# Kernel tuning notes

Measured on AMD Instinct MI355X. Metric: run time of the kernel, lower is better.

The kernel has to match this reference:

```python
import jax, jax.numpy as jnp
import numpy as np

B, T, C, H = 4, 2048, 512, 8
HS = C // H  # head_size = 64
EPS = 1e-5


def layernorm(x, g, b):
    mu = jnp.mean(x, axis=-1, keepdims=True)
    var = jnp.mean(jnp.square(x - mu), axis=-1, keepdims=True)
    return (x - mu) * jax.lax.rsqrt(var + EPS) * g + b


def setup_inputs() -> dict:
    key = jax.random.key(0)
    ks = jax.random.split(key, 12)
    s_attn = 1.0 / np.sqrt(C)
    s_ff1 = 1.0 / np.sqrt(C)
    s_ff2 = 1.0 / np.sqrt(4 * C)
    return {
        "x": jax.random.normal(ks[0], (B, T, C), jnp.float32),
        "wq": jax.random.normal(ks[1], (H, C, HS), jnp.float32) * s_attn,
        "wk": jax.random.normal(ks[2], (H, C, HS), jnp.float32) * s_attn,
        "wv": jax.random.normal(ks[3], (H, C, HS), jnp.float32) * s_attn,
        "w1": jax.random.normal(ks[4], (C, 4 * C), jnp.float32) * s_ff1,
        "b1": jnp.zeros((4 * C,), jnp.float32),
        "w2": jax.random.normal(ks[5], (4 * C, C), jnp.float32) * s_ff2,
        "b2": jnp.zeros((C,), jnp.float32),
        "ln1_g": jnp.ones((C,), jnp.float32),
        "ln1_b": jnp.zeros((C,), jnp.float32),
        "ln2_g": jnp.ones((C,), jnp.float32),
        "ln2_b": jnp.zeros((C,), jnp.float32),
    }


def reference(x, wq, wk, wv, w1, b1, w2, b2, ln1_g, ln1_b, ln2_g, ln2_b):
    # pre-LN multi-head causal self-attention
    h = layernorm(x, ln1_g, ln1_b)                       # [B,T,C]
    q = jnp.einsum("btc,hcd->bhtd", h, wq)
    k = jnp.einsum("btc,hcd->bhtd", h, wk)
    v = jnp.einsum("btc,hcd->bhtd", h, wv)
    # NOTE: source scales by full embed dim C, not head_size
    scores = jnp.einsum("bhtd,bhsd->bhts", q, k) * (C ** -0.5)  # [B,H,T,T]
    causal = jnp.tril(jnp.ones((T, T), bool))
    scores = jnp.where(causal, scores, -jnp.inf)
    att = jax.nn.softmax(scores, axis=-1)
    out = jnp.einsum("bhts,bhsd->bhtd", att, v)          # [B,H,T,HS]
    out = out.transpose(0, 2, 1, 3).reshape(B, T, C)     # concat heads
    x = x + out
    # FFN with residual
    h2 = layernorm(x, ln2_g, ln2_b)
    ff = jax.nn.relu(h2 @ w1 + b1) @ w2 + b2
    return x + ff
```

## Files before the change

kernel.cpp:

```cpp
#include <hip/hip_runtime.h>

typedef unsigned short ushort_t;
typedef __attribute__((ext_vector_type(8))) short short8;
typedef __attribute__((ext_vector_type(4))) float floatx4;

#define B_  4
#define T_  2048
#define C_  512
#define H_  8
#define HS_ 64
#define M_  (B_*T_)
#define SCALE2 0.06376140168547404f

__device__ __forceinline__ float b2f(ushort_t u) {
  union { unsigned int i; float f; } w; w.i = ((unsigned int)u) << 16; return w.f;
}
__device__ __forceinline__ ushort_t f2b(float f) {
  union { float f; unsigned int i; } w; w.f = f;
  unsigned int x = w.i;
  return (ushort_t)((x + 0x7fffu + ((x >> 16) & 1u)) >> 16);
}
__device__ __forceinline__ ushort_t f2b_fast(float f) {
  union { float f; unsigned int i; } w; w.f = f;
  return (ushort_t)((w.i + 0x8000u) >> 16);
}
__device__ __forceinline__ void gl_lds16(const ushort_t* g, ushort_t* l) {
  __builtin_amdgcn_global_load_lds((const unsigned int*)g, (unsigned int*)l, 16, 0, 0);
}

__global__ __launch_bounds__(256) void transpose_all(const float* __restrict__ wq,
                                                     const float* __restrict__ wk,
                                                     const float* __restrict__ wv,
                                                     const float* __restrict__ w1,
                                                     const float* __restrict__ w2,
                                                     ushort_t* __restrict__ qkvt,
                                                     ushort_t* __restrict__ w1t,
                                                     ushort_t* __restrict__ w2t) {
  __shared__ ushort_t t[32][33];
  int idx = blockIdx.x;
  const float* in; ushort_t* out; int K, N, bx, by, z = 0;
  if (idx < 768) {
    int seg = idx >> 8, li = idx & 255;
    in = seg == 0 ? wq : (seg == 1 ? wk : wv);
    out = qkvt + (size_t)seg * 262144;
    K = 512; N = 64;
    z = li >> 5; li &= 31;
    bx = li & 1; by = li >> 1;
  } else if (idx < 1792) {
    int li = idx - 768;
    in = w1; out = w1t; K = 512; N = 2048;
    bx = li & 63; by = li >> 6;
  } else {
    int li = idx - 1792;
    in = w2; out = w2t; K = 2048; N = 512;
    bx = li & 15; by = li >> 4;
  }
  size_t zoff = (size_t)z * K * N;
  int n0 = bx * 32, k0 = by * 32;
  int tx = threadIdx.x & 31, ty = threadIdx.x >> 5;
#pragma unroll
  for (int i = 0; i < 4; i++)
    t[ty + 8 * i][tx] = f2b(in[zoff + (size_t)(k0 + ty + 8 * i) * N + n0 + tx]);
  __syncthreads();
#pragma unroll
  for (int i = 0; i < 4; i++)
    out[zoff + (size_t)(n0 + ty + 8 * i) * K + k0 + tx] = t[tx][ty + 8 * i];
}

__global__ __launch_bounds__(256) void ln_k(const float* __restrict__ X,
                                            const float* __restrict__ g,
                                            const float* __restrict__ bb,
                                            ushort_t* __restrict__ Y) {
  int wave = threadIdx.x >> 6, lane = threadIdx.x & 63;
  size_t row = (size_t)blockIdx.x * 4 + wave;
  float v[8], s = 0.f, s2 = 0.f;
#pragma unroll
  for (int i = 0; i < 8; i++) {
    float x = X[row * C_ + lane + 64 * i];
    v[i] = x; s += x; s2 += x * x;
  }
#pragma unroll
  for (int off = 32; off >= 1; off >>= 1) {
    s += __shfl_xor(s, off); s2 += __shfl_xor(s2, off);
  }
  float mu = s * (1.0f / C_);
  float var = s2 * (1.0f / C_) - mu * mu;
  float rs = rsqrtf(var + 1e-5f);
  ushort_t* yr = Y + row * C_;
#pragma unroll
  for (int i = 0; i < 8; i++) {
    int c = lane + 64 * i;
    yr[c] = f2b((v[i] - mu) * rs * g[c] + bb[c]);
  }
}

__global__ __launch_bounds__(256) void gemm_bt128(const ushort_t* __restrict__ A,
                                                  const ushort_t* __restrict__ Bt,
                                                  ushort_t* __restrict__ Out,
                                                  int K, int ldOut,
                                                  const float* __restrict__ bias,
                                                  int relu) {
  __shared__ __align__(16) ushort_t As[128 * 64];
  __shared__ __align__(16) ushort_t Bs[128 * 64];
  const int tid = threadIdx.x;
  const int lane = tid & 63, wave = tid >> 6;
  const long row0 = (long)blockIdx.y * 128;
  const long col0 = (long)blockIdx.x * 128;
  const int srow = wave * 32 + (lane >> 3);
  const int scol = (((lane & 7) ^ ((lane >> 3) & 7))) * 8;
  const ushort_t* Ab = A + (size_t)(row0 + srow) * K + scol;
  const ushort_t* Bb = Bt + (size_t)(col0 + srow) * K + scol;
  const int wm = (wave >> 1) * 64, wn = (wave & 1) * 64;
  const int fq = lane >> 4, fl = lane & 15;
  floatx4 acc[4][4] = {};

  for (int k0 = 0; k0 < K; k0 += 64) {
    __syncthreads();
#pragma unroll
    for (int i = 0; i < 4; i++) {
      gl_lds16(Ab + (size_t)(i * 8) * K + k0, &As[(wave * 32 + i * 8) * 64]);
      gl_lds16(Bb + (size_t)(i * 8) * K + k0, &Bs[(wave * 32 + i * 8) * 64]);
    }
    __syncthreads();
#pragma unroll
    for (int ks = 0; ks < 2; ks++) {
      short8 af[4], bf[4];
      const int sl = ((ks * 4 + fq) ^ (fl & 7)) * 8;
#pragma unroll
      for (int i = 0; i < 4; i++) {
        af[i] = *(const short8*)&As[(wm + i * 16 + fl) * 64 + sl];
        bf[i] = *(const short8*)&Bs[(wn + i * 16 + fl) * 64 + sl];
      }
#pragma unroll
      for (int fi = 0; fi < 4; fi++)
#pragma unroll
        for (int fj = 0; fj < 4; fj++)
          acc[fi][fj] = __builtin_amdgcn_mfma_f32_16x16x32_bf16(af[fi], bf[fj], acc[fi][fj], 0, 0, 0);
    }
  }
#pragma unroll
  for (int fi = 0; fi < 4; fi++)
#pragma unroll
    for (int fj = 0; fj < 4; fj++) {
      long gcol = col0 + wn + fj * 16 + fl;
      float bv = bias ? bias[gcol] : 0.0f;
#pragma unroll
      for (int r = 0; r < 4; r++) {
        long grow = row0 + wm + fi * 16 + fq * 4 + r;
        float v = acc[fi][fj][r] + bv;
        if (relu) v = fmaxf(v, 0.0f);
        Out[(size_t)grow * ldOut + gcol] = f2b(v);
      }
    }
}

__global__ __launch_bounds__(256) void gemm_bt64(const ushort_t* __restrict__ A,
                                                 const ushort_t* __restrict__ Bt,
                                                 float* __restrict__ Out,
                                                 int K, int ldOut,
                                                 const float* __restrict__ bias,
                                                 const float* __restrict__ residual) {
  __shared__ __align__(16) ushort_t As[64 * 64];
  __shared__ __align__(16) ushort_t Bs[64 * 64];
  const int tid = threadIdx.x;
  const int lane = tid & 63, wave = tid >> 6;
  const long row0 = (long)blockIdx.y * 64;
  const long col0 = (long)blockIdx.x * 64;
  const int srow = wave * 16 + (lane >> 3);
  const int scol = (((lane & 7) ^ ((lane >> 3) & 7))) * 8;
  const ushort_t* Ab = A + (size_t)(row0 + srow) * K + scol;
  const ushort_t* Bb = Bt + (size_t)(col0 + srow) * K + scol;
  const int wm = (wave >> 1) * 32, wn = (wave & 1) * 32;
  const int fq = lane >> 4, fl = lane & 15;
  floatx4 acc[2][2] = {};

  for (int k0 = 0; k0 < K; k0 += 64) {
    __syncthreads();
#pragma unroll
    for (int i = 0; i < 2; i++) {
      gl_lds16(Ab + (size_t)(i * 8) * K + k0, &As[(wave * 16 + i * 8) * 64]);
      gl_lds16(Bb + (size_t)(i * 8) * K + k0, &Bs[(wave * 16 + i * 8) * 64]);
    }
    __syncthreads();
#pragma unroll
    for (int ks = 0; ks < 2; ks++) {
      short8 af[2], bf[2];
      const int sl = ((ks * 4 + fq) ^ (fl & 7)) * 8;
#pragma unroll
      for (int i = 0; i < 2; i++) {
        af[i] = *(const short8*)&As[(wm + i * 16 + fl) * 64 + sl];
        bf[i] = *(const short8*)&Bs[(wn + i * 16 + fl) * 64 + sl];
      }
#pragma unroll
      for (int fi = 0; fi < 2; fi++)
#pragma unroll
        for (int fj = 0; fj < 2; fj++)
          acc[fi][fj] = __builtin_amdgcn_mfma_f32_16x16x32_bf16(af[fi], bf[fj], acc[fi][fj], 0, 0, 0);
    }
  }
#pragma unroll
  for (int fi = 0; fi < 2; fi++)
#pragma unroll
    for (int fj = 0; fj < 2; fj++) {
      long gcol = col0 + wn + fj * 16 + fl;
      float bv = bias[gcol];
#pragma unroll
      for (int r = 0; r < 4; r++) {
        long grow = row0 + wm + fi * 16 + fq * 4 + r;
        size_t oi = (size_t)grow * ldOut + gcol;
        Out[oi] = acc[fi][fj][r] + bv + residual[oi];
      }
    }
}

__global__ __launch_bounds__(256) void flash_attn(const ushort_t* __restrict__ QKV,
                                                  const float* __restrict__ X,
                                                  float* __restrict__ X1) {
  __shared__ __align__(16) ushort_t kt[64 * 72];
  __shared__ __align__(16) ushort_t vt[80 * 72];
  __shared__ __align__(16) ushort_t pt[64 * 72];
  const int tid = threadIdx.x;
  const int lane = tid & 63, wave = tid >> 6;
  const int fq = lane >> 4, fl = lane & 15;
  const int qt_idx = (T_ / 64 - 1) - (blockIdx.x >> 5);
  const int bh = blockIdx.x & 31;
  const int h = bh & 7, b = bh >> 3;
  const int hoff = h * HS_;
  const int q0 = qt_idx * 64;
  const int LD = 3 * C_;

  for (int i = tid; i < 16 * 72; i += 256) {
    int rr = i / 72, cc = i % 72;
    vt[(64 + rr) * 72 + cc] = (rr == 0) ? (ushort_t)0x3F80 : (ushort_t)0;
  }

  short8 qf0, qf1;
  {
    const ushort_t* qp = QKV + (size_t)((size_t)b * T_ + q0 + wave * 16 + fl) * LD + hoff + fq * 8;
    qf0 = *(const short8*)(qp);
    qf1 = *(const short8*)(qp + 32);
  }
  floatx4 oacc[4] = {};
  floatx4 lacc = {};

  const int sr = (tid >> 3) * 2;
  const int d0 = (tid & 7) * 8;
  const ushort_t* kbase = QKV + (size_t)((size_t)b * T_ + sr) * LD + hoff + C_;

  short8 k0v = *(const short8*)(kbase + d0);
  short8 k1v = *(const short8*)(kbase + LD + d0);
  short8 v0v = *(const short8*)(kbase + C_ + d0);
  short8 v1v = *(const short8*)(kbase + C_ + LD + d0);

  for (int st = 0; st <= qt_idx; st++) {
    __syncthreads();
    *(short8*)&kt[sr * 72 + d0] = k0v;
    *(short8*)&kt[(sr + 1) * 72 + d0] = k1v;
#pragma unroll
    for (int i = 0; i < 8; i++) {
      int d = d0 + i;
      int scol = sr ^ (8 * (d >> 3));
      unsigned int pk = ((unsigned int)(ushort_t)v0v[i]) |
                        (((unsigned int)(ushort_t)v1v[i]) << 16);
      *(unsigned int*)&vt[d * 72 + scol] = pk;
    }
    __syncthreads();

    if (st < qt_idx) {
      const ushort_t* kp = kbase + (size_t)(st + 1) * 64 * LD;
      k0v = *(const short8*)(kp + d0);
      k1v = *(const short8*)(kp + LD + d0);
      v0v = *(const short8*)(kp + C_ + d0);
      v1v = *(const short8*)(kp + C_ + LD + d0);
    }

    int s0 = st * 64;
    floatx4 sacc[4] = {};
#pragma unroll
    for (int fn = 0; fn < 4; fn++) {
      short8 kf0 = *(const short8*)&kt[(fn * 16 + fl) * 72 + fq * 8];
      short8 kf1 = *(const short8*)&kt[(fn * 16 + fl) * 72 + 32 + fq * 8];
      sacc[fn] = __builtin_amdgcn_mfma_f32_16x16x32_bf16(qf0, kf0, sacc[fn], 0, 0, 0);
      sacc[fn] = __builtin_amdgcn_mfma_f32_16x16x32_bf16(qf1, kf1, sacc[fn], 0, 0, 0);
    }
    bool diag = (st == qt_idx);
#pragma unroll
    for (int fn = 0; fn < 4; fn++)
#pragma unroll
      for (int r = 0; r < 4; r++) {
        int qg = q0 + wave * 16 + fq * 4 + r;
        float p = exp2f(sacc[fn][r] * SCALE2);
        if (diag && (s0 + fn * 16 + fl) > qg) p = 0.0f;
        pt[(wave * 16 + fq * 4 + r) * 72 + fn * 16 + fl] = f2b_fast(p);
      }
    short8 pf0 = *(const short8*)&pt[(wave * 16 + fl) * 72 + fq * 8];
    short8 pf1 = *(const short8*)&pt[(wave * 16 + fl) * 72 + 32 + fq * 8];
#pragma unroll
    for (int fn = 0; fn < 4; fn++) {
      int drow = fn * 16 + fl;
      int sw = 8 * (drow >> 3);
      short8 vf0 = *(const short8*)&vt[drow * 72 + ((fq * 8) ^ sw)];
      short8 vf1 = *(const short8*)&vt[drow * 72 + ((32 + fq * 8) ^ sw)];
      oacc[fn] = __builtin_amdgcn_mfma_f32_16x16x32_bf16(pf0, vf0, oacc[fn], 0, 0, 0);
      oacc[fn] = __builtin_amdgcn_mfma_f32_16x16x32_bf16(pf1, vf1, oacc[fn], 0, 0, 0);
    }
    {
      short8 of0 = *(const short8*)&vt[(64 + fl) * 72 + fq * 8];
      short8 of1 = *(const short8*)&vt[(64 + fl) * 72 + 32 + fq * 8];
      lacc = __builtin_amdgcn_mfma_f32_16x16x32_bf16(pf0, of0, lacc, 0, 0, 0);
      lacc = __builtin_amdgcn_mfma_f32_16x16x32_bf16(pf1, of1, lacc, 0, 0, 0);
    }
  }
#pragma unroll
  for (int r = 0; r < 4; r++) {
    float lr = __shfl(lacc[r], lane & 48);
    float inv = 1.0f / lr;
    int qg = q0 + wave * 16 + fq * 4 + r;
#pragma unroll
    for (int fn = 0; fn < 4; fn++) {
      int d = fn * 16 + fl;
      size_t oi = ((size_t)b * T_ + qg) * C_ + hoff + d;
      X1[oi] = oacc[fn][r] * inv + X[oi];
    }
  }
}

extern "C" void kernel_launch(void* const* d_in, const int* in_sizes, int n_in,
                              void* d_out, int out_size, void* d_ws, size_t ws_size,
                              hipStream_t stream) {
  const float* x  = (const float*)d_in[0];
  const float* wq = (const float*)d_in[1];
  const float* wk = (const float*)d_in[2];
  const float* wv = (const float*)d_in[3];
  const float* w1 = (const float*)d_in[4];
  const float* b1 = (const float*)d_in[5];
  const float* w2 = (const float*)d_in[6];
  const float* b2 = (const float*)d_in[7];
  const float* ln1g = (const float*)d_in[8];
  const float* ln1b = (const float*)d_in[9];
  const float* ln2g = (const float*)d_in[10];
  const float* ln2b = (const float*)d_in[11];
  ushort_t* ws = (ushort_t*)d_ws;

  const size_t SZ = (size_t)M_ * C_;
  ushort_t* qkvt = ws;
  ushort_t* w1t  = qkvt + 786432;
  ushort_t* w2t  = w1t + 1048576;
  ushort_t* qkv  = w2t + 1048576;
  ushort_t* h2   = qkv;
  ushort_t* ff1  = qkv + SZ;
  ushort_t* h    = (ushort_t*)d_out;
  float* x1      = (float*)d_out;
  float* outf    = (float*)d_out;

  transpose_all<<<2816, 256, 0, stream>>>(wq, wk, wv, w1, w2, qkvt, w1t, w2t);
  ln_k<<<M_ / 4, 256, 0, stream>>>(x, ln1g, ln1b, h);
  gemm_bt128<<<dim3(12, 64), 256, 0, stream>>>(h, qkvt, qkv, 512, 1536, nullptr, 0);
  flash_attn<<<B_ * H_ * (T_ / 64), 256, 0, stream>>>(qkv, x, x1);
  ln_k<<<M_ / 4, 256, 0, stream>>>(x1, ln2g, ln2b, h2);
  for (int p = 0; p < 2; p++) {
    const size_t roff = (size_t)p * 4096;
    gemm_bt128<<<dim3(16, 32), 256, 0, stream>>>(h2 + roff * C_, w1t, ff1,
                                                 512, 2048, b1, 1);
    gemm_bt64<<<dim3(8, 64), 256, 0, stream>>>(ff1, w2t, outf + roff * C_,
                                               2048, 512, b2, x1 + roff * C_);
  }
}
```

Measured before the change: 248.5 us.

## Use 128-query attention tiles with split K/V loaders and swap GEMM grid order

Flash attention now handles 128 query rows per 512-thread block, so each K/V tile staged in shared memory is reused by eight waves instead of four. Half the threads load K and half load V, which halves the per-thread global load work. Tiles are ordered long-first, and the first wave half skips the final diagonal step. Separately, all GEMM launches swap grid x/y so consecutive blocks walk along rows sharing one weight column tile, which changes L2 reuse. The attention change leaves fewer blocks (512) and raises LDS use per block, which may reduce occupancy.

```diff
diff --git a/kernel.cpp b/kernel.cpp
--- a/kernel.cpp
+++ b/kernel.cpp
@@ -104,8 +104,8 @@
   __shared__ __align__(16) ushort_t Bs[128 * 64];
   const int tid = threadIdx.x;
   const int lane = tid & 63, wave = tid >> 6;
-  const long row0 = (long)blockIdx.y * 128;
-  const long col0 = (long)blockIdx.x * 128;
+  const long row0 = (long)blockIdx.x * 128;
+  const long col0 = (long)blockIdx.y * 128;
   const int srow = wave * 32 + (lane >> 3);
   const int scol = (((lane & 7) ^ ((lane >> 3) & 7))) * 8;
   const ushort_t* Ab = A + (size_t)(row0 + srow) * K + scol;
@@ -164,8 +164,8 @@
   __shared__ __align__(16) ushort_t Bs[64 * 64];
   const int tid = threadIdx.x;
   const int lane = tid & 63, wave = tid >> 6;
-  const long row0 = (long)blockIdx.y * 64;
-  const long col0 = (long)blockIdx.x * 64;
+  const long row0 = (long)blockIdx.x * 64;
+  const long col0 = (long)blockIdx.y * 64;
   const int srow = wave * 16 + (lane >> 3);
   const int scol = (((lane & 7) ^ ((lane >> 3) & 7))) * 8;
   const ushort_t* Ab = A + (size_t)(row0 + srow) * K + scol;
@@ -213,25 +213,28 @@
     }
 }
 
-__global__ __launch_bounds__(256) void flash_attn(const ushort_t* __restrict__ QKV,
+__global__ __launch_bounds__(512) void flash_attn(const ushort_t* __restrict__ QKV,
                                                   const float* __restrict__ X,
                                                   float* __restrict__ X1) {
   __shared__ __align__(16) ushort_t kt[64 * 72];
   __shared__ __align__(16) ushort_t vt[80 * 72];
-  __shared__ __align__(16) ushort_t pt[64 * 72];
+  __shared__ __align__(16) ushort_t pt[128 * 72];
   const int tid = threadIdx.x;
   const int lane = tid & 63, wave = tid >> 6;
   const int fq = lane >> 4, fl = lane & 15;
-  const int qt_idx = (T_ / 64 - 1) - (blockIdx.x >> 5);
+  const int g = blockIdx.x >> 5;
+  const int tile = g < 8 ? 15 - g : g - 8;
   const int bh = blockIdx.x & 31;
   const int h = bh & 7, b = bh >> 3;
   const int hoff = h * HS_;
-  const int q0 = qt_idx * 64;
+  const int q0 = tile * 128;
   const int LD = 3 * C_;
-
-  for (int i = tid; i < 16 * 72; i += 256) {
-    int rr = i / 72, cc = i % 72;
-    vt[(64 + rr) * 72 + cc] = (rr == 0) ? (ushort_t)0x3F80 : (ushort_t)0;
+  const int nst = 2 * tile + 2;
+  const int whalf = wave >> 2;
+
+  for (int i = tid; i < 16 * 72; i += 512) {
+    int rr = i / 72;
+    vt[(64 + rr) * 72 + (i % 72)] = (rr == 0) ? (ushort_t)0x3F80 : (ushort_t)0;
   }
 
   short8 qf0, qf1;
@@ -243,72 +246,76 @@
   floatx4 oacc[4] = {};
   floatx4 lacc = {};
 
-  const int sr = (tid >> 3) * 2;
-  const int d0 = (tid & 7) * 8;
-  const ushort_t* kbase = QKV + (size_t)((size_t)b * T_ + sr) * LD + hoff + C_;
-
-  short8 k0v = *(const short8*)(kbase + d0);
-  short8 k1v = *(const short8*)(kbase + LD + d0);
-  short8 v0v = *(const short8*)(kbase + C_ + d0);
-  short8 v1v = *(const short8*)(kbase + C_ + LD + d0);
-
-  for (int st = 0; st <= qt_idx; st++) {
-    __syncthreads();
-    *(short8*)&kt[sr * 72 + d0] = k0v;
-    *(short8*)&kt[(sr + 1) * 72 + d0] = k1v;
-#pragma unroll
-    for (int i = 0; i < 8; i++) {
-      int d = d0 + i;
-      int scol = sr ^ (8 * (d >> 3));
-      unsigned int pk = ((unsigned int)(ushort_t)v0v[i]) |
-                        (((unsigned int)(ushort_t)v1v[i]) << 16);
-      *(unsigned int*)&vt[d * 72 + scol] = pk;
-    }
-    __syncthreads();
-
-    if (st < qt_idx) {
-      const ushort_t* kp = kbase + (size_t)(st + 1) * 64 * LD;
-      k0v = *(const short8*)(kp + d0);
-      k1v = *(const short8*)(kp + LD + d0);
-      v0v = *(const short8*)(kp + C_ + d0);
-      v1v = *(const short8*)(kp + C_ + LD + d0);
-    }
-
-    int s0 = st * 64;
-    floatx4 sacc[4] = {};
-#pragma unroll
-    for (int fn = 0; fn < 4; fn++) {
-      short8 kf0 = *(const short8*)&kt[(fn * 16 + fl) * 72 + fq * 8];
-      short8 kf1 = *(const short8*)&kt[(fn * 16 + fl) * 72 + 32 + fq * 8];
-      sacc[fn] = __builtin_amdgcn_mfma_f32_16x16x32_bf16(qf0, kf0, sacc[fn], 0, 0, 0);
-      sacc[fn] = __builtin_amdgcn_mfma_f32_16x16x32_bf16(qf1, kf1, sacc[fn], 0, 0, 0);
-    }
-    bool diag = (st == qt_idx);
-#pragma unroll
-    for (int fn = 0; fn < 4; fn++)
-#pragma unroll
-      for (int r = 0; r < 4; r++) {
-        int qg = q0 + wave * 16 + fq * 4 + r;
-        float p = exp2f(sacc[fn][r] * SCALE2);
-        if (diag && (s0 + fn * 16 + fl) > qg) p = 0.0f;
-        pt[(wave * 16 + fq * 4 + r) * 72 + fn * 16 + fl] = f2b_fast(p);
-      }
-    short8 pf0 = *(const short8*)&pt[(wave * 16 + fl) * 72 + fq * 8];
-    short8 pf1 = *(const short8*)&pt[(wave * 16 + fl) * 72 + 32 + fq * 8];
-#pragma unroll
-    for (int fn = 0; fn < 4; fn++) {
-      int drow = fn * 16 + fl;
-      int sw = 8 * (drow >> 3);
-      short8 vf0 = *(const short8*)&vt[drow * 72 + ((fq * 8) ^ sw)];
-      short8 vf1 = *(const short8*)&vt[drow * 72 + ((32 + fq * 8) ^ sw)];
-      oacc[fn] = __builtin_amdgcn_mfma_f32_16x16x32_bf16(pf0, vf0, oacc[fn], 0, 0, 0);
-      oacc[fn] = __builtin_amdgcn_mfma_f32_16x16x32_bf16(pf1, vf1, oacc[fn], 0, 0, 0);
-    }
-    {
-      short8 of0 = *(const short8*)&vt[(64 + fl) * 72 + fq * 8];
-      short8 of1 = *(const short8*)&vt[(64 + fl) * 72 + 32 + fq * 8];
-      lacc = __builtin_amdgcn_mfma_f32_16x16x32_bf16(pf0, of0, lacc, 0, 0, 0);
-      lacc = __builtin_amdgcn_mfma_f32_16x16x32_bf16(pf1, of1, lacc, 0, 0, 0);
+  const int role = tid >> 8;
+  const int t2 = tid & 255;
+  const int sr2 = (t2 >> 3) * 2;
+  const int d0 = (t2 & 7) * 8;
+  const ushort_t* sbase = QKV + (size_t)((size_t)b * T_ + sr2) * LD + hoff +
+                          (role ? C_ : 2 * C_);
+
+  short8 r0 = *(const short8*)(sbase + d0);
+  short8 r1 = *(const short8*)(sbase + LD + d0);
+
+  for (int st = 0; st < nst; st++) {
+    __syncthreads();
+    if (role) {
+      *(short8*)&kt[sr2 * 72 + d0] = r0;
+      *(short8*)&kt[(sr2 + 1) * 72 + d0] = r1;
+    } else {
+#pragma unroll
+      for (int i = 0; i < 8; i++) {
+        int d = d0 + i;
+        int scol = sr2 ^ (8 * (d >> 3));
+        unsigned int pk = ((unsigned int)(ushort_t)r0[i]) |
+                          (((unsigned int)(ushort_t)r1[i]) << 16);
+        *(unsigned int*)&vt[d * 72 + scol] = pk;
+      }
+    }
+    __syncthreads();
+
+    if (st < nst - 1) {
+      const ushort_t* sp = sbase + (size_t)(st + 1) * 64 * LD;
+      r0 = *(const short8*)(sp + d0);
+      r1 = *(const short8*)(sp + LD + d0);
+    }
+
+    if (!(whalf == 0 && st == nst - 1)) {
+      int s0 = st * 64;
+      floatx4 sacc[4] = {};
+#pragma unroll
+      for (int fn = 0; fn < 4; fn++) {
+        short8 kf0 = *(const short8*)&kt[(fn * 16 + fl) * 72 + fq * 8];
+        short8 kf1 = *(const short8*)&kt[(fn * 16 + fl) * 72 + 32 + fq * 8];
+        sacc[fn] = __builtin_amdgcn_mfma_f32_16x16x32_bf16(qf0, kf0, sacc[fn], 0, 0, 0);
+        sacc[fn] = __builtin_amdgcn_mfma_f32_16x16x32_bf16(qf1, kf1, sacc[fn], 0, 0, 0);
+      }
+      bool diag = (st == 2 * tile + whalf);
+#pragma unroll
+      for (int fn = 0; fn < 4; fn++)
+#pragma unroll
+        for (int r = 0; r < 4; r++) {
+          int qg = q0 + wave * 16 + fq * 4 + r;
+          float p = exp2f(sacc[fn][r] * SCALE2);
+          if (diag && (s0 + fn * 16 + fl) > qg) p = 0.0f;
+          pt[(wave * 16 + fq * 4 + r) * 72 + fn * 16 + fl] = f2b_fast(p);
+        }
+      short8 pf0 = *(const short8*)&pt[(wave * 16 + fl) * 72 + fq * 8];
+      short8 pf1 = *(const short8*)&pt[(wave * 16 + fl) * 72 + 32 + fq * 8];
+#pragma unroll
+      for (int fn = 0; fn < 4; fn++) {
+        int drow = fn * 16 + fl;
+        int sw = 8 * (drow >> 3);
+        short8 vf0 = *(const short8*)&vt[drow * 72 + ((fq * 8) ^ sw)];
+        short8 vf1 = *(const short8*)&vt[drow * 72 + ((32 + fq * 8) ^ sw)];
+        oacc[fn] = __builtin_amdgcn_mfma_f32_16x16x32_bf16(pf0, vf0, oacc[fn], 0, 0, 0);
+        oacc[fn] = __builtin_amdgcn_mfma_f32_16x16x32_bf16(pf1, vf1, oacc[fn], 0, 0, 0);
+      }
+      {
+        short8 of0 = *(const short8*)&vt[(64 + fl) * 72 + fq * 8];
+        short8 of1 = *(const short8*)&vt[(64 + fl) * 72 + 32 + fq * 8];
+        lacc = __builtin_amdgcn_mfma_f32_16x16x32_bf16(pf0, of0, lacc, 0, 0, 0);
+        lacc = __builtin_amdgcn_mfma_f32_16x16x32_bf16(pf1, of1, lacc, 0, 0, 0);
+      }
     }
   }
 #pragma unroll
@@ -355,14 +362,14 @@
 
   transpose_all<<<2816, 256, 0, stream>>>(wq, wk, wv, w1, w2, qkvt, w1t, w2t);
   ln_k<<<M_ / 4, 256, 0, stream>>>(x, ln1g, ln1b, h);
-  gemm_bt128<<<dim3(12, 64), 256, 0, stream>>>(h, qkvt, qkv, 512, 1536, nullptr, 0);
-  flash_attn<<<B_ * H_ * (T_ / 64), 256, 0, stream>>>(qkv, x, x1);
+  gemm_bt128<<<dim3(64, 12), 256, 0, stream>>>(h, qkvt, qkv, 512, 1536, nullptr, 0);
+  flash_attn<<<B_ * H_ * (T_ / 128), 512, 0, stream>>>(qkv, x, x1);
   ln_k<<<M_ / 4, 256, 0, stream>>>(x1, ln2g, ln2b, h2);
   for (int p = 0; p < 2; p++) {
     const size_t roff = (size_t)p * 4096;
-    gemm_bt128<<<dim3(16, 32), 256, 0, stream>>>(h2 + roff * C_, w1t, ff1,
+    gemm_bt128<<<dim3(32, 16), 256, 0, stream>>>(h2 + roff * C_, w1t, ff1,
                                                  512, 2048, b1, 1);
-    gemm_bt64<<<dim3(8, 64), 256, 0, stream>>>(ff1, w2t, outf + roff * C_,
+    gemm_bt64<<<dim3(64, 8), 256, 0, stream>>>(ff1, w2t, outf + roff * C_,
                                                2048, 512, b2, x1 + roff * C_);
   }
 }
```

Result: no change. 247.0 us (-0.6%).
